# Kernel tuning notes

Measured on AMD Instinct MI355X. Metric: run time of the kernel, lower is better.

Reference implementation:

```python
import jax, jax.numpy as jnp
import numpy as np

BN_EPS = 1e-5


def setup_inputs() -> dict:
    key = jax.random.key(0)
    ks = jax.random.split(key, 12)
    B, N, S, D1, D2 = 2, 16384, 4096, 128, 256
    C1, C2 = 256, 128  # mlp channels
    return {
        "xyz1": jax.random.normal(ks[0], (B, 3, N), dtype=jnp.float32),
        "xyz2": jax.random.normal(ks[1], (B, 3, S), dtype=jnp.float32),
        "points1": jax.random.normal(ks[2], (B, D1, N), dtype=jnp.float32),
        "points2": jax.random.normal(ks[3], (B, D2, S), dtype=jnp.float32),
        "w1": jax.random.normal(ks[4], (D1 + D2, C1), dtype=jnp.float32) * 0.05,
        "b1": jax.random.normal(ks[5], (C1,), dtype=jnp.float32) * 0.05,
        "g1": jax.random.uniform(ks[6], (C1,), dtype=jnp.float32, minval=0.5, maxval=1.5),
        "beta1": jax.random.normal(ks[7], (C1,), dtype=jnp.float32) * 0.05,
        "w2": jax.random.normal(ks[8], (C1, C2), dtype=jnp.float32) * 0.05,
        "b2": jax.random.normal(ks[9], (C2,), dtype=jnp.float32) * 0.05,
        "g2": jax.random.uniform(ks[10], (C2,), dtype=jnp.float32, minval=0.5, maxval=1.5),
        "beta2": jax.random.normal(ks[11], (C2,), dtype=jnp.float32) * 0.05,
    }


def _conv_bn_relu(x, W, b, g, beta):
    # 1x1 Conv1d == per-point matmul; BatchNorm1d training-mode stats over (B, N).
    y = x @ W + b                              # [B, N, Cout]
    mu = jnp.mean(y, axis=(0, 1))
    var = jnp.var(y, axis=(0, 1))              # biased variance, matches torch BN
    y = g * (y - mu) * jax.lax.rsqrt(var + BN_EPS) + beta
    return jax.nn.relu(y)


def reference(xyz1, xyz2, points1, points2, w1, b1, g1, beta1, w2, b2, g2, beta2):
    x1 = jnp.transpose(xyz1, (0, 2, 1))        # [B, N, 3]
    x2 = jnp.transpose(xyz2, (0, 2, 1))        # [B, S, 3]
    p2 = jnp.transpose(points2, (0, 2, 1))     # [B, S, D2]

    # squared pairwise distance [B, N, S], clamped at 0
    d = (jnp.sum(x1 ** 2, axis=-1, keepdims=True)
         - 2.0 * jnp.einsum('bnc,bsc->bns', x1, x2)
         + jnp.sum(x2 ** 2, axis=-1)[:, None, :])
    d = jnp.maximum(d, 0.0)

    # 3 nearest neighbors (ascending smallest distances) -- same math as full sort + slice
    neg_d3, idx = jax.lax.top_k(-d, 3)         # [B, N, 3]
    d3 = jnp.maximum(-neg_d3, 1e-6)
    recip = 1.0 / d3
    w = recip / jnp.maximum(jnp.sum(recip, axis=-1, keepdims=True), 1e-6)

    nb = jax.vmap(lambda p, i: p[i])(p2, idx)  # [B, N, 3, D2]
    interp = jnp.sum(nb * w[..., None], axis=2)
    interp = jnp.nan_to_num(interp, nan=0.0, posinf=0.0, neginf=0.0)

    p1 = jnp.transpose(points1, (0, 2, 1))     # [B, N, D1]
    x = jnp.concatenate([p1, interp], axis=-1) # [B, N, D1+D2]

    x = _conv_bn_relu(x, w1, b1, g1, beta1)
    x = _conv_bn_relu(x, w2, b2, g2, beta2)
    x = jnp.nan_to_num(x, nan=0.0, posinf=0.0, neginf=0.0)
    return jnp.transpose(x, (0, 2, 1))         # [B, C2, N]
```

## Files before the change

### kernel.cpp

```cpp
#include <hip/hip_runtime.h>

#define B_   2
#define N_   16384
#define S_   4096
#define D1_  128
#define D2_  256
#define C1_  256
#define C2_  128
#define M_   (B_ * N_)

typedef __bf16 bf16_t;
typedef bf16_t bf16x8 __attribute__((ext_vector_type(8)));
typedef bf16_t bf16x4 __attribute__((ext_vector_type(4)));
typedef float  f32x4  __attribute__((ext_vector_type(4)));

__device__ __forceinline__ void gload16(const void* g, void* l) {
  __builtin_amdgcn_global_load_lds(
      (const __attribute__((address_space(1))) void*)g,
      (__attribute__((address_space(3))) void*)l, 16, 0, 0);
}

__device__ __forceinline__ float med3f(float a, float b, float c) {
  float d;
  asm("v_med3_f32 %0, %1, %2, %3" : "=v"(d) : "v"(a), "v"(b), "v"(c));
  return d;
}

__global__ __launch_bounds__(256) void setup_k(const float* __restrict__ points2,
                                               const float* __restrict__ points1,
                                               const float* __restrict__ w1,
                                               const float* __restrict__ w2,
                                               const float* __restrict__ xyz2,
                                               float* __restrict__ p2t,
                                               bf16_t* __restrict__ X,
                                               bf16_t* __restrict__ w1t,
                                               bf16_t* __restrict__ w2t,
                                               float4* __restrict__ c4) {
  __shared__ float tile[32][33];
  int bi = blockIdx.x, t = threadIdx.x;
  int tx = t & 31, ty = t >> 5;
  if (bi < 2048) {
    int b = bi >> 10, rest = bi & 1023;
    int s0 = (rest & 127) * 32, c0 = (rest >> 7) * 32;
    const float* src = points2 + (size_t)b * D2_ * S_;
#pragma unroll
    for (int k = 0; k < 4; ++k)
      tile[ty + k * 8][tx] = src[(size_t)(c0 + ty + k * 8) * S_ + s0 + tx];
    __syncthreads();
    float* dst = p2t + (size_t)b * S_ * D2_;
#pragma unroll
    for (int k = 0; k < 4; ++k)
      dst[(size_t)(s0 + ty + k * 8) * D2_ + c0 + tx] = tile[tx][ty + k * 8];
  } else if (bi < 6144) {
    int bj = bi - 2048;
    int b = bj >> 11, rest = bj & 2047;
    int n0 = (rest & 511) * 32, c0 = (rest >> 9) * 32;
    const float* src = points1 + (size_t)b * D1_ * N_;
#pragma unroll
    for (int k = 0; k < 4; ++k)
      tile[ty + k * 8][tx] = src[(size_t)(c0 + ty + k * 8) * N_ + n0 + tx];
    __syncthreads();
#pragma unroll
    for (int k = 0; k < 4; ++k)
      X[(size_t)(b * N_ + n0 + ty + k * 8) * 384 + c0 + tx] = (bf16_t)tile[tx][ty + k * 8];
  } else {
    int i = (bi - 6144) * 256 + t;
    if (i < C1_ * 384) {
      int n = i / 384, k = i % 384;
      w1t[i] = (bf16_t)w1[(size_t)k * C1_ + n];
    } else if (i < C1_ * 384 + C2_ * C1_) {
      int j = i - C1_ * 384;
      int n = j / C1_, k = j % C1_;
      w2t[j] = (bf16_t)w2[(size_t)k * C2_ + n];
    } else {
      int j = i - (C1_ * 384 + C2_ * C1_);
      if (j < B_ * S_) {
        int b = j >> 12, s = j & (S_ - 1);
        const float* X2p = xyz2 + (size_t)b * 3 * S_;
        float x = X2p[s], y = X2p[S_ + s], z = X2p[2 * S_ + s];
        c4[j] = make_float4(-2.f * x, -2.f * y, -2.f * z, x * x + y * y + z * z);
      }
    }
  }
}

__global__ __launch_bounds__(512) void knn_k(const float* __restrict__ xyz1,
                                             const float4* __restrict__ c4,
                                             const float* __restrict__ p2t,
                                             bf16_t* __restrict__ X) {
  __shared__ char lds[65536];
  int t = threadIdx.x, l = t & 63, w = t >> 6;
  int b  = blockIdx.x >> 8;
  int nb = (blockIdx.x & 255) * 64;
  const float4* cb = c4 + (size_t)b * S_;
#pragma unroll
  for (int k = 0; k < 8; ++k)
    gload16(cb + t + 512 * k, lds + (size_t)(t + 512 * k) * 16);
  int n = nb + l;
  const float* X1 = xyz1 + (size_t)b * 3 * N_;
  float ax = X1[n], ay = X1[N_ + n], az = X1[2 * N_ + n];
  float negp = -(ax * ax + ay * ay + az * az);
  __syncthreads();
  const float4* cc = (const float4*)lds + w * 512;
  int base = w * 512;
  float m0 = 3e38f, m1 = 3e38f, m2 = 3e38f;
  int   j0 = 0, j1 = 0, j2 = 0;
#pragma unroll 4
  for (int i = 0; i < 512; ++i) {
    float4 c = cc[i];
    float v = c.w;
    v = fmaf(az, c.z, v);
    v = fmaf(ay, c.y, v);
    v = fmaf(ax, c.x, v);
    v = fmaxf(v, negp);
    int idx = base + i;
    bool b0 = v < m0, b1 = v < m1, b2 = v < m2;
    float nm0 = fminf(v, m0);
    float nm1 = med3f(m0, v, m1);
    float nm2 = med3f(m1, v, m2);
    j2 = b1 ? j1 : (b2 ? idx : j2);
    j1 = b0 ? j0 : (b1 ? idx : j1);
    j0 = b0 ? idx : j0;
    m0 = nm0; m1 = nm1; m2 = nm2;
  }
  __syncthreads();
  float* SV = (float*)lds;
  int*   SI = (int*)(lds + 6144);
  float* QW = (float*)(lds + 12288);
  int*   QI = (int*)(lds + 13056);
  SV[(w * 3 + 0) * 64 + l] = m0;  SV[(w * 3 + 1) * 64 + l] = m1;  SV[(w * 3 + 2) * 64 + l] = m2;
  SI[(w * 3 + 0) * 64 + l] = j0;  SI[(w * 3 + 1) * 64 + l] = j1;  SI[(w * 3 + 2) * 64 + l] = j2;
  __syncthreads();
  if (t < 64) {
    float M0 = 3e38f, M1 = 3e38f, M2 = 3e38f;
    int   a0 = 0, a1 = 0, a2 = 0;
    for (int ch = 0; ch < 8; ++ch)
#pragma unroll
      for (int k = 0; k < 3; ++k) {
        float v = SV[(ch * 3 + k) * 64 + t];
        int  ix = SI[(ch * 3 + k) * 64 + t];
        bool b0 = v < M0, b1 = v < M1, b2 = v < M2;
        float nm0 = fminf(v, M0);
        float nm1 = med3f(M0, v, M1);
        float nm2 = med3f(M1, v, M2);
        a2 = b1 ? a1 : (b2 ? ix : a2);
        a1 = b0 ? a0 : (b1 ? ix : a1);
        a0 = b0 ? ix : a0;
        M0 = nm0; M1 = nm1; M2 = nm2;
      }
    float p  = -negp;
    float d0 = fmaxf(p + M0, 1e-6f);
    float d1 = fmaxf(p + M1, 1e-6f);
    float d2 = fmaxf(p + M2, 1e-6f);
    float r0 = 1.f / d0, r1 = 1.f / d1, r2 = 1.f / d2;
    float dn = fmaxf(r0 + r1 + r2, 1e-6f);
    QW[t * 3 + 0] = r0 / dn;  QW[t * 3 + 1] = r1 / dn;  QW[t * 3 + 2] = r2 / dn;
    QI[t * 3 + 0] = a0;       QI[t * 3 + 1] = a1;       QI[t * 3 + 2] = a2;
  }
  __syncthreads();
  int q  = t >> 3, sg = (t & 7) * 32;
  float w0 = QW[q * 3 + 0], w1 = QW[q * 3 + 1], w2 = QW[q * 3 + 2];
  int   i0 = QI[q * 3 + 0], i1 = QI[q * 3 + 1], i2 = QI[q * 3 + 2];
  const float* pb = p2t + (size_t)b * S_ * D2_;
  const float4* r0p = (const float4*)(pb + (size_t)i0 * D2_ + sg);
  const float4* r1p = (const float4*)(pb + (size_t)i1 * D2_ + sg);
  const float4* r2p = (const float4*)(pb + (size_t)i2 * D2_ + sg);
  size_t row = (size_t)b * N_ + nb + q;
  bf16_t* xo = X + row * 384 + 128 + sg;
#pragma unroll
  for (int it = 0; it < 8; ++it) {
    float4 A = r0p[it], Bv = r1p[it], Cv = r2p[it];
    bf16x4 o;
    o[0] = (bf16_t)(w0 * A.x + w1 * Bv.x + w2 * Cv.x);
    o[1] = (bf16_t)(w0 * A.y + w1 * Bv.y + w2 * Cv.y);
    o[2] = (bf16_t)(w0 * A.z + w1 * Bv.z + w2 * Cv.z);
    o[3] = (bf16_t)(w0 * A.w + w1 * Bv.w + w2 * Cv.w);
    *(bf16x4*)&xo[it * 4] = o;
  }
}

__global__ __launch_bounds__(256) void gemm1_k(const bf16_t* __restrict__ A,
                                               const bf16_t* __restrict__ Bt,
                                               const float* __restrict__ bias,
                                               bf16_t* __restrict__ Y,
                                               float* __restrict__ st) {
  const int K = 384;
  __shared__ bf16_t As[128 * 32];
  __shared__ bf16_t Bs[128 * 32];
  int tid = threadIdx.x, lane = tid & 63, w = tid >> 6;
  int wr = w >> 1, wc = w & 1;
  int m0 = blockIdx.x * 128, n0 = blockIdx.y * 128;
  int e0 = (w * 2 + 0) * 512 + lane * 8;
  int e1 = (w * 2 + 1) * 512 + lane * 8;
  int ra0 = e0 >> 5, ca0 = e0 & 31;
  int ra1 = e1 >> 5, ca1 = e1 & 31;
  f32x4 acc[4][4];
  f32x4 z = {0.f, 0.f, 0.f, 0.f};
#pragma unroll
  for (int i = 0; i < 4; ++i)
#pragma unroll
    for (int j = 0; j < 4; ++j) acc[i][j] = z;
  for (int k0 = 0; k0 < K; k0 += 32) {
    __syncthreads();
    gload16(A + (size_t)(m0 + ra0) * K + k0 + ca0, &As[e0]);
    gload16(A + (size_t)(m0 + ra1) * K + k0 + ca1, &As[e1]);
    gload16(Bt + (size_t)(n0 + ra0) * K + k0 + ca0, &Bs[e0]);
    gload16(Bt + (size_t)(n0 + ra1) * K + k0 + ca1, &Bs[e1]);
    __syncthreads();
    bf16x8 af[4], bfr[4];
    int arow = wr * 64 + (lane & 15);
    int brow = wc * 64 + (lane & 15);
    int kc = 8 * (lane >> 4);
#pragma unroll
    for (int i = 0; i < 4; ++i) af[i]  = *(const bf16x8*)&As[(arow + i * 16) * 32 + kc];
#pragma unroll
    for (int j = 0; j < 4; ++j) bfr[j] = *(const bf16x8*)&Bs[(brow + j * 16) * 32 + kc];
#pragma unroll
    for (int i = 0; i < 4; ++i)
#pragma unroll
      for (int j = 0; j < 4; ++j)
        acc[i][j] = __builtin_amdgcn_mfma_f32_16x16x32_bf16(af[i], bfr[j], acc[i][j], 0, 0, 0);
  }
#pragma unroll
  for (int j = 0; j < 4; ++j) {
    int col = n0 + wc * 64 + j * 16 + (lane & 15);
    float bv = bias[col];
    float sj = 0.f, ssj = 0.f;
#pragma unroll
    for (int i = 0; i < 4; ++i) {
      int r = m0 + wr * 64 + i * 16 + ((lane >> 4) << 2);
#pragma unroll
      for (int q = 0; q < 4; ++q) {
        float y = acc[i][j][q] + bv;
        Y[(size_t)(r + q) * C1_ + col] = (bf16_t)y;
        sj += y; ssj += y * y;
      }
    }
    sj  += __shfl_xor(sj, 16);  sj  += __shfl_xor(sj, 32);
    ssj += __shfl_xor(ssj, 16); ssj += __shfl_xor(ssj, 32);
    if ((lane >> 4) == 0) {
      atomicAdd(&st[col], sj);
      atomicAdd(&st[C1_ + col], ssj);
    }
  }
}

__global__ __launch_bounds__(256) void bn1apply_k(const bf16_t* __restrict__ Y,
                                                  const float* __restrict__ st,
                                                  const float* __restrict__ g,
                                                  const float* __restrict__ be,
                                                  bf16_t* __restrict__ X2) {
  __shared__ float sa[256], sb[256];
  int t = threadIdx.x;
  {
    const float invM = 1.f / (float)M_;
    float mu  = st[t] * invM;
    float var = fmaxf(st[C1_ + t] * invM - mu * mu, 0.f);
    float a = g[t] * rsqrtf(var + 1e-5f);
    sa[t] = a;
    sb[t] = be[t] - mu * a;
  }
  __syncthreads();
  int cc = (t & 31) * 8;
  float a[8], s[8];
#pragma unroll
  for (int u = 0; u < 8; ++u) { a[u] = sa[cc + u]; s[u] = sb[cc + u]; }
  int r0 = blockIdx.x * 64 + (t >> 5);
  for (int it = 0; it < 8; ++it) {
    int r = r0 + it * 8;
    bf16x8 v = *(const bf16x8*)&Y[(size_t)r * C1_ + cc];
    bf16x8 o;
#pragma unroll
    for (int u = 0; u < 8; ++u) {
      float f = (float)v[u];
      f = fmaxf(a[u] * f + s[u], 0.f);
      o[u] = (bf16_t)f;
    }
    *(bf16x8*)&X2[(size_t)r * C1_ + cc] = o;
  }
}

__global__ __launch_bounds__(256) void gemm2_k(const bf16_t* __restrict__ A,
                                               const bf16_t* __restrict__ Bt,
                                               const float* __restrict__ bias,
                                               float* __restrict__ OUT,
                                               float* __restrict__ st) {
  const int K = 256;
  __shared__ bf16_t As[128 * 32];
  __shared__ bf16_t Bs[128 * 32];
  int tid = threadIdx.x, lane = tid & 63, w = tid >> 6;
  int wr = w >> 1, wc = w & 1;
  int m0 = blockIdx.x * 128;
  int e0 = (w * 2 + 0) * 512 + lane * 8;
  int e1 = (w * 2 + 1) * 512 + lane * 8;
  int ra0 = e0 >> 5, ca0 = e0 & 31;
  int ra1 = e1 >> 5, ca1 = e1 & 31;
  f32x4 acc[4][4];
  f32x4 z = {0.f, 0.f, 0.f, 0.f};
#pragma unroll
  for (int i = 0; i < 4; ++i)
#pragma unroll
    for (int j = 0; j < 4; ++j) acc[i][j] = z;
  for (int k0 = 0; k0 < K; k0 += 32) {
    __syncthreads();
    gload16(A + (size_t)(m0 + ra0) * K + k0 + ca0, &As[e0]);
    gload16(A + (size_t)(m0 + ra1) * K + k0 + ca1, &As[e1]);
    gload16(Bt + (size_t)ra0 * K + k0 + ca0, &Bs[e0]);
    gload16(Bt + (size_t)ra1 * K + k0 + ca1, &Bs[e1]);
    __syncthreads();
    bf16x8 af[4], bfr[4];
    int arow = wr * 64 + (lane & 15);
    int brow = wc * 64 + (lane & 15);
    int kc = 8 * (lane >> 4);
#pragma unroll
    for (int i = 0; i < 4; ++i) af[i]  = *(const bf16x8*)&As[(arow + i * 16) * 32 + kc];
#pragma unroll
    for (int j = 0; j < 4; ++j) bfr[j] = *(const bf16x8*)&Bs[(brow + j * 16) * 32 + kc];
#pragma unroll
    for (int i = 0; i < 4; ++i)
#pragma unroll
      for (int j = 0; j < 4; ++j)
        acc[i][j] = __builtin_amdgcn_mfma_f32_16x16x32_bf16(af[i], bfr[j], acc[i][j], 0, 0, 0);
  }
#pragma unroll
  for (int j = 0; j < 4; ++j) {
    int col = wc * 64 + j * 16 + (lane & 15);
    float bv = bias[col];
    float sj = 0.f, ssj = 0.f;
#pragma unroll
    for (int i = 0; i < 4; ++i) {
      int r  = m0 + wr * 64 + i * 16 + ((lane >> 4) << 2);
      int bb = r >> 14, n = r & (N_ - 1);
      f32x4 v = acc[i][j];
#pragma unroll
      for (int q = 0; q < 4; ++q) {
        v[q] += bv;
        sj += v[q]; ssj += v[q] * v[q];
      }
      *(f32x4*)&OUT[((size_t)(bb * C2_ + col)) * N_ + n] = v;
    }
    sj  += __shfl_xor(sj, 16);  sj  += __shfl_xor(sj, 32);
    ssj += __shfl_xor(ssj, 16); ssj += __shfl_xor(ssj, 32);
    if ((lane >> 4) == 0) {
      atomicAdd(&st[col], sj);
      atomicAdd(&st[C2_ + col], ssj);
    }
  }
}

__global__ __launch_bounds__(256) void bn2apply_k(float* __restrict__ OUT,
                                                  const float* __restrict__ st,
                                                  const float* __restrict__ g,
                                                  const float* __restrict__ be) {
  __shared__ float ab[2];
  int t = threadIdx.x;
  int c = (blockIdx.x >> 4) & 127;
  if (t == 0) {
    const float invM = 1.f / (float)M_;
    float mu  = st[c] * invM;
    float var = fmaxf(st[C2_ + c] * invM - mu * mu, 0.f);
    float a = g[c] * rsqrtf(var + 1e-5f);
    ab[0] = a;
    ab[1] = be[c] - mu * a;
  }
  __syncthreads();
  float a = ab[0], s = ab[1];
  size_t i4 = (size_t)blockIdx.x * 256 + t;
  f32x4 v = *(f32x4*)&OUT[i4 * 4];
#pragma unroll
  for (int u = 0; u < 4; ++u) v[u] = fmaxf(a * v[u] + s, 0.f);
  *(f32x4*)&OUT[i4 * 4] = v;
}

extern "C" void kernel_launch(void* const* d_in, const int* in_sizes, int n_in,
                              void* d_out, int out_size, void* d_ws, size_t ws_size,
                              hipStream_t stream) {
  const float* xyz1    = (const float*)d_in[0];
  const float* xyz2    = (const float*)d_in[1];
  const float* points1 = (const float*)d_in[2];
  const float* points2 = (const float*)d_in[3];
  const float* w1      = (const float*)d_in[4];
  const float* b1      = (const float*)d_in[5];
  const float* g1      = (const float*)d_in[6];
  const float* beta1   = (const float*)d_in[7];
  const float* w2      = (const float*)d_in[8];
  const float* b2      = (const float*)d_in[9];
  const float* g2      = (const float*)d_in[10];
  const float* beta2   = (const float*)d_in[11];
  float* out = (float*)d_out;

  char* p = (char*)d_ws;
  size_t off = 0;
  bf16_t* w1t = (bf16_t*)(p + off); off += (size_t)C1_ * 384 * 2;
  bf16_t* w2t = (bf16_t*)(p + off); off += (size_t)C2_ * C1_ * 2;
  float*  p2t = (float*)(p + off);  off += (size_t)B_ * S_ * D2_ * 4;
  bf16_t* X   = (bf16_t*)(p + off); off += (size_t)M_ * 384 * 2;
  bf16_t* Y1  = (bf16_t*)(p + off); off += (size_t)M_ * C1_ * 2;
  bf16_t* X2  = (bf16_t*)(p + off); off += (size_t)M_ * C1_ * 2;
  float4* C4  = (float4*)(p + off); off += (size_t)B_ * S_ * 16;
  float*  ST1 = (float*)(p + off);  off += 2048;
  float*  ST2 = (float*)(p + off);  off += 1024;

  hipMemsetAsync(ST1, 0, 3072, stream);

  setup_k<<<6688, 256, 0, stream>>>(points2, points1, w1, w2, xyz2, p2t, X, w1t, w2t, C4);
  knn_k<<<512, 512, 0, stream>>>(xyz1, C4, p2t, X);
  gemm1_k<<<dim3(M_ / 128, 2), 256, 0, stream>>>(X, w1t, b1, Y1, ST1);
  bn1apply_k<<<512, 256, 0, stream>>>(Y1, ST1, g1, beta1, X2);
  gemm2_k<<<M_ / 128, 256, 0, stream>>>(X2, w2t, b2, out, ST2);
  bn2apply_k<<<4096, 256, 0, stream>>>(out, ST2, g2, beta2);
}
```

Baseline: 151.7 us.

## Split KNN work across more blocks with smaller staged candidate chunks

The KNN kernel now handles 32 query points per block instead of 64, with 16 candidate slices per query, and launches 1024 blocks. Candidate coordinates are staged through a 16KB LDS buffer in four rounds rather than one 64KB load, which lowers LDS use per block so more blocks can be resident. The top-3 merge becomes a two-level reduction. This adds extra block-wide barriers, and each thread in the gather stage now handles 16 channels instead of 32.

```diff
diff --git a/kernel.cpp b/kernel.cpp
--- a/kernel.cpp
+++ b/kernel.cpp
@@ -84,61 +84,68 @@
   }
 }
 
-__global__ __launch_bounds__(512) void knn_k(const float* __restrict__ xyz1,
-                                             const float4* __restrict__ c4,
-                                             const float* __restrict__ p2t,
-                                             bf16_t* __restrict__ X) {
-  __shared__ char lds[65536];
+__global__ __launch_bounds__(512, 8) void knn_k(const float* __restrict__ xyz1,
+                                                const float4* __restrict__ c4,
+                                                const float* __restrict__ p2t,
+                                                bf16_t* __restrict__ X) {
+  __shared__ float4 cbuf[1024];
+  __shared__ float  T3V[2][3][32];
+  __shared__ int    T3I[2][3][32];
+  __shared__ float  QWs[32][3];
+  __shared__ int    QIs[32][3];
   int t = threadIdx.x, l = t & 63, w = t >> 6;
-  int b  = blockIdx.x >> 8;
-  int nb = (blockIdx.x & 255) * 64;
-  const float4* cb = c4 + (size_t)b * S_;
-#pragma unroll
-  for (int k = 0; k < 8; ++k)
-    gload16(cb + t + 512 * k, lds + (size_t)(t + 512 * k) * 16);
-  int n = nb + l;
+  int q = l & 31, h = l >> 5;
+  int s = w * 2 + h;
+  int b  = blockIdx.x >> 9;
+  int nb = (blockIdx.x & 511) * 32;
+  int n  = nb + q;
   const float* X1 = xyz1 + (size_t)b * 3 * N_;
   float ax = X1[n], ay = X1[N_ + n], az = X1[2 * N_ + n];
   float negp = -(ax * ax + ay * ay + az * az);
-  __syncthreads();
-  const float4* cc = (const float4*)lds + w * 512;
-  int base = w * 512;
+  const float4* cb = c4 + (size_t)b * S_;
   float m0 = 3e38f, m1 = 3e38f, m2 = 3e38f;
   int   j0 = 0, j1 = 0, j2 = 0;
+  for (int r = 0; r < 4; ++r) {
+    __syncthreads();
+    gload16(cb + r * 1024 + t,       (char*)cbuf + (size_t)t * 16);
+    gload16(cb + r * 1024 + t + 512, (char*)cbuf + (size_t)(t + 512) * 16);
+    __syncthreads();
+    const float4* cs = cbuf + s * 64;
+    int base = r * 1024 + s * 64;
 #pragma unroll 4
-  for (int i = 0; i < 512; ++i) {
-    float4 c = cc[i];
-    float v = c.w;
-    v = fmaf(az, c.z, v);
-    v = fmaf(ay, c.y, v);
-    v = fmaf(ax, c.x, v);
-    v = fmaxf(v, negp);
-    int idx = base + i;
-    bool b0 = v < m0, b1 = v < m1, b2 = v < m2;
-    float nm0 = fminf(v, m0);
-    float nm1 = med3f(m0, v, m1);
-    float nm2 = med3f(m1, v, m2);
-    j2 = b1 ? j1 : (b2 ? idx : j2);
-    j1 = b0 ? j0 : (b1 ? idx : j1);
-    j0 = b0 ? idx : j0;
-    m0 = nm0; m1 = nm1; m2 = nm2;
-  }
-  __syncthreads();
-  float* SV = (float*)lds;
-  int*   SI = (int*)(lds + 6144);
-  float* QW = (float*)(lds + 12288);
-  int*   QI = (int*)(lds + 13056);
-  SV[(w * 3 + 0) * 64 + l] = m0;  SV[(w * 3 + 1) * 64 + l] = m1;  SV[(w * 3 + 2) * 64 + l] = m2;
-  SI[(w * 3 + 0) * 64 + l] = j0;  SI[(w * 3 + 1) * 64 + l] = j1;  SI[(w * 3 + 2) * 64 + l] = j2;
+    for (int i = 0; i < 64; ++i) {
+      float4 c = cs[i];
+      float v = c.w;
+      v = fmaf(az, c.z, v);
+      v = fmaf(ay, c.y, v);
+      v = fmaf(ax, c.x, v);
+      v = fmaxf(v, negp);
+      int idx = base + i;
+      bool b0 = v < m0, b1 = v < m1, b2 = v < m2;
+      float nm0 = fminf(v, m0);
+      float nm1 = med3f(m0, v, m1);
+      float nm2 = med3f(m1, v, m2);
+      j2 = b1 ? j1 : (b2 ? idx : j2);
+      j1 = b0 ? j0 : (b1 ? idx : j1);
+      j0 = b0 ? idx : j0;
+      m0 = nm0; m1 = nm1; m2 = nm2;
+    }
+  }
+  __syncthreads();
+  float* SV = (float*)cbuf;
+  int*   SI = (int*)cbuf + 1536;
+  SV[(s * 3 + 0) * 32 + q] = m0;  SV[(s * 3 + 1) * 32 + q] = m1;  SV[(s * 3 + 2) * 32 + q] = m2;
+  SI[(s * 3 + 0) * 32 + q] = j0;  SI[(s * 3 + 1) * 32 + q] = j1;  SI[(s * 3 + 2) * 32 + q] = j2;
   __syncthreads();
   if (t < 64) {
+    int th = t >> 5, tq = t & 31;
     float M0 = 3e38f, M1 = 3e38f, M2 = 3e38f;
     int   a0 = 0, a1 = 0, a2 = 0;
-    for (int ch = 0; ch < 8; ++ch)
+    for (int s2 = th * 8; s2 < th * 8 + 8; ++s2)
 #pragma unroll
       for (int k = 0; k < 3; ++k) {
-        float v = SV[(ch * 3 + k) * 64 + t];
-        int  ix = SI[(ch * 3 + k) * 64 + t];
+        float v = SV[(s2 * 3 + k) * 32 + tq];
+        int  ix = SI[(s2 * 3 + k) * 32 + tq];
         bool b0 = v < M0, b1 = v < M1, b2 = v < M2;
         float nm0 = fminf(v, M0);
         float nm1 = med3f(M0, v, M1);
@@ -148,34 +155,52 @@
         a0 = b0 ? ix : a0;
         M0 = nm0; M1 = nm1; M2 = nm2;
       }
+    T3V[th][0][tq] = M0; T3V[th][1][tq] = M1; T3V[th][2][tq] = M2;
+    T3I[th][0][tq] = a0; T3I[th][1][tq] = a1; T3I[th][2][tq] = a2;
+  }
+  __syncthreads();
+  if (t < 32) {
+    float M0 = T3V[0][0][t], M1 = T3V[0][1][t], M2 = T3V[0][2][t];
+    int   a0 = T3I[0][0][t], a1 = T3I[0][1][t], a2 = T3I[0][2][t];
+#pragma unroll
+    for (int k = 0; k < 3; ++k) {
+      float v = T3V[1][k][t];
+      int  ix = T3I[1][k][t];
+      bool b0 = v < M0, b1 = v < M1, b2 = v < M2;
+      float nm0 = fminf(v, M0);
+      float nm1 = med3f(M0, v, M1);
+      float nm2 = med3f(M1, v, M2);
+      a2 = b1 ? a1 : (b2 ? ix : a2);
+      a1 = b0 ? a0 : (b1 ? ix : a1);
+      a0 = b0 ? ix : a0;
+      M0 = nm0; M1 = nm1; M2 = nm2;
+    }
     float p  = -negp;
     float d0 = fmaxf(p + M0, 1e-6f);
     float d1 = fmaxf(p + M1, 1e-6f);
     float d2 = fmaxf(p + M2, 1e-6f);
     float r0 = 1.f / d0, r1 = 1.f / d1, r2 = 1.f / d2;
     float dn = fmaxf(r0 + r1 + r2, 1e-6f);
-    QW[t * 3 + 0] = r0 / dn;  QW[t * 3 + 1] = r1 / dn;  QW[t * 3 + 2] = r2 / dn;
-    QI[t * 3 + 0] = a0;       QI[t * 3 + 1] = a1;       QI[t * 3 + 2] = a2;
-  }
-  __syncthreads();
-  int q  = t >> 3, sg = (t & 7) * 32;
-  float w0 = QW[q * 3 + 0], w1 = QW[q * 3 + 1], w2 = QW[q * 3 + 2];
-  int   i0 = QI[q * 3 + 0], i1 = QI[q * 3 + 1], i2 = QI[q * 3 + 2];
+    QWs[t][0] = r0 / dn;  QWs[t][1] = r1 / dn;  QWs[t][2] = r2 / dn;
+    QIs[t][0] = a0;       QIs[t][1] = a1;       QIs[t][2] = a2;
+  }
+  __syncthreads();
+  int gq = t >> 4, c0 = (t & 15) * 16;
+  float w0 = QWs[gq][0], w1 = QWs[gq][1], w2 = QWs[gq][2];
+  int   i0 = QIs[gq][0], i1 = QIs[gq][1], i2 = QIs[gq][2];
   const float* pb = p2t + (size_t)b * S_ * D2_;
-  const float4* r0p = (const float4*)(pb + (size_t)i0 * D2_ + sg);
-  const float4* r1p = (const float4*)(pb + (size_t)i1 * D2_ + sg);
-  const float4* r2p = (const float4*)(pb + (size_t)i2 * D2_ + sg);
-  size_t row = (size_t)b * N_ + nb + q;
-  bf16_t* xo = X + row * 384 + 128 + sg;
-#pragma unroll
-  for (int it = 0; it < 8; ++it) {
-    float4 A = r0p[it], Bv = r1p[it], Cv = r2p[it];
+  bf16_t* xo = X + ((size_t)(b * N_ + nb + gq)) * 384 + 128 + c0;
+#pragma unroll
+  for (int u = 0; u < 4; ++u) {
+    float4 A  = *(const float4*)(pb + (size_t)i0 * D2_ + c0 + u * 4);
+    float4 Bv = *(const float4*)(pb + (size_t)i1 * D2_ + c0 + u * 4);
+    float4 Cv = *(const float4*)(pb + (size_t)i2 * D2_ + c0 + u * 4);
     bf16x4 o;
     o[0] = (bf16_t)(w0 * A.x + w1 * Bv.x + w2 * Cv.x);
     o[1] = (bf16_t)(w0 * A.y + w1 * Bv.y + w2 * Cv.y);
     o[2] = (bf16_t)(w0 * A.z + w1 * Bv.z + w2 * Cv.z);
     o[3] = (bf16_t)(w0 * A.w + w1 * Bv.w + w2 * Cv.w);
-    *(bf16x4*)&xo[it * 4] = o;
+    *(bf16x4*)&xo[u * 4] = o;
   }
 }
 
@@ -404,7 +429,7 @@
   hipMemsetAsync(ST1, 0, 3072, stream);
 
   setup_k<<<6688, 256, 0, stream>>>(points2, points1, w1, w2, xyz2, p2t, X, w1t, w2t, C4);
-  knn_k<<<512, 512, 0, stream>>>(xyz1, C4, p2t, X);
+  knn_k<<<1024, 512, 0, stream>>>(xyz1, C4, p2t, X);
   gemm1_k<<<dim3(M_ / 128, 2), 256, 0, stream>>>(X, w1t, b1, Y1, ST1);
   bn1apply_k<<<512, 256, 0, stream>>>(Y1, ST1, g1, beta1, X2);
   gemm2_k<<<M_ / 128, 256, 0, stream>>>(X2, w2t, b2, out, ST2);
```

Result: faster. 144.0 us (-5.1%).
